# Performance work log

Hardware: AMD Instinct MI355X
Metric: run time of the kernel (lower is better)

## Reference

```python
import jax, jax.numpy as jnp
import numpy as np

N_KERNELS = 5
MUL_FACTOR = 2.0
# 2.0 ** (arange(5) - 2) = [0.25, 0.5, 1, 2, 4]
BANDWIDTH_MULTIPLIERS = MUL_FACTOR ** (np.arange(N_KERNELS) - N_KERNELS // 2)


def setup_inputs() -> dict:
    key = jax.random.key(0)
    kx, ky = jax.random.split(key)
    X = jax.random.normal(kx, (4096, 256), dtype=jnp.float32)
    Y = jax.random.normal(ky, (4096, 256), dtype=jnp.float32)
    return {"X": X, "Y": Y}


def _pairwise_sq_dists(Z):
    # ||z_i - z_j||^2 via GEMM; clamp tiny negatives from roundoff.
    sq = jnp.sum(Z * Z, axis=-1)  # [2N]
    d2 = sq[:, None] + sq[None, :] - 2.0 * (Z @ Z.T)  # [2N, 2N]
    return jnp.maximum(d2, 0.0)


def reference(X, Y):
    n = X.shape[0]
    Z = jnp.concatenate([X, Y], axis=0)  # [2N, D]
    d2 = _pairwise_sq_dists(Z)  # [2N, 2N]
    n_samples = d2.shape[0]
    # bandwidth uses .data in torch -> detached
    bandwidth = jax.lax.stop_gradient(d2.sum()) / (n_samples ** 2 - n_samples)
    mults = jnp.asarray(BANDWIDTH_MULTIPLIERS, dtype=d2.dtype)  # [5]
    # K = sum_k exp(-d2 / (bandwidth * mult_k))
    K = jnp.exp(-d2[None, :, :] / (bandwidth * mults)[:, None, None]).sum(axis=0)
    XX = K[:n, :n].mean()
    XY = K[:n, n:].mean()
    YY = K[n:, n:].mean()
    return XX - 2.0 * XY + YY
```

## Files before the change

### kernel.cpp

```cpp
#include <hip/hip_runtime.h>
#include <math.h>


#define N_HALF 4096
#define DIM 256
#define M_TOT 8192
#define TILE 128
#define NT 64
#define NT_HALF 32
#define CHUNK 4
#define NCHUNK 520

typedef unsigned short ushort_t;
typedef __attribute__((ext_vector_type(8))) short short8;
typedef __attribute__((ext_vector_type(4))) float floatx4;

__device__ ushort_t g_zf[M_TOT * DIM];

__device__ __forceinline__ ushort_t f2bf(float f) {
    unsigned u = __float_as_uint(f);
    u += 0x7fffu + ((u >> 16) & 1u);
    return (ushort_t)(u >> 16);
}

__device__ __forceinline__ void gload_lds16(const ushort_t* g, ushort_t* l) {
    __builtin_amdgcn_global_load_lds(
        (const __attribute__((address_space(1))) void*)g,
        (__attribute__((address_space(3))) void*)l, 16, 0, 0);
}

__device__ __forceinline__ void stage_slice(const ushort_t* gA, const ushort_t* gB,
                                            ushort_t* lA, ushort_t* lB,
                                            int wave, int lane) {
#pragma unroll
    for (int i = 0; i < 2; ++i) {
        const int c = wave * 2 + i;
        gload_lds16(gA + (size_t)c * 4096 + lane * 8, lA + c * 512);
        gload_lds16(gB + (size_t)c * 4096 + lane * 8, lB + c * 512);
    }
}

__device__ __forceinline__ void compute_kk(const ushort_t* lA, const ushort_t* lB,
                                           int a0, int b0, int laneoff,
                                           floatx4 (&accv)[4][4]) {
    short8 af[4], bf[4];
#pragma unroll
    for (int mi = 0; mi < 4; ++mi)
        af[mi] = *(const short8*)(lA + (a0 + mi) * 512 + laneoff);
#pragma unroll
    for (int ni = 0; ni < 4; ++ni)
        bf[ni] = *(const short8*)(lB + (b0 + ni) * 512 + laneoff);
#pragma unroll
    for (int mi = 0; mi < 4; ++mi)
#pragma unroll
        for (int ni = 0; ni < 4; ++ni)
            accv[mi][ni] = __builtin_amdgcn_mfma_f32_16x16x32_bf16(
                af[mi], bf[ni], accv[mi][ni], 0, 0, 0);
}

__global__ __launch_bounds__(256) void k_prep(const float* __restrict__ X,
                                              const float* __restrict__ Y,
                                              float* __restrict__ sq,
                                              float* __restrict__ colsum_r,
                                              float* __restrict__ Ssum_r) {
    __shared__ float cpart[4][256];
    __shared__ float spart[4];
    const int t = threadIdx.x, wave = t >> 6, lane = t & 63;
    const int row0 = blockIdx.x * 16 + wave * 4;
    const int kk = lane >> 3, q = (lane >> 1) & 3, j0 = (lane & 1) * 4;
    float c0 = 0.f, c1 = 0.f, c2 = 0.f, c3 = 0.f, ssum = 0.f;
#pragma unroll
    for (int i = 0; i < 4; ++i) {
        const int row = row0 + i;
        const float* p = (row < N_HALF) ? (X + (size_t)row * DIM)
                                        : (Y + (size_t)(row - N_HALF) * DIM);
        const float4 v = *((const float4*)p + lane);
        ushort4 hi;
        hi.x = f2bf(v.x); hi.y = f2bf(v.y); hi.z = f2bf(v.z); hi.w = f2bf(v.w);
        const int rb = row >> 4, m = row & 15;
        *(ushort4*)(g_zf + (size_t)rb * 4096 + kk * 512 + m * 32 + q * 8 + j0) = hi;
        c0 += v.x; c1 += v.y; c2 += v.z; c3 += v.w;
        float s = fmaf(v.x, v.x, fmaf(v.y, v.y, fmaf(v.z, v.z, v.w * v.w)));
#pragma unroll
        for (int off = 32; off > 0; off >>= 1) s += __shfl_xor(s, off);
        if (lane == 0) sq[row] = s;
        ssum += s;
    }
    float4 cp; cp.x = c0; cp.y = c1; cp.z = c2; cp.w = c3;
    *(float4*)&cpart[wave][lane * 4] = cp;
    if (lane == 0) spart[wave] = ssum;
    __syncthreads();
    const float cs = cpart[0][t] + cpart[1][t] + cpart[2][t] + cpart[3][t];
    const int rep = blockIdx.x & 7;
    atomicAdd(&colsum_r[rep * 256 + t], cs);
    if (t == 0) atomicAdd(&Ssum_r[rep], spart[0] + spart[1] + spart[2] + spart[3]);
}

__global__ __launch_bounds__(256) void k_bw(const float* __restrict__ colsum_r,
                                            const float* __restrict__ Ssum_r,
                                            float* __restrict__ c2out) {
    __shared__ double sred[4];
    const int t = threadIdx.x, lane = t & 63, wave = t >> 6;
    float csf = 0.f;
#pragma unroll
    for (int r = 0; r < 8; ++r) csf += colsum_r[r * 256 + t];
    double p = (double)csf * (double)csf;
#pragma unroll
    for (int off = 32; off > 0; off >>= 1) p += __shfl_xor(p, off);
    if (lane == 0) sred[wave] = p;
    __syncthreads();
    if (t == 0) {
        const double SS = sred[0] + sred[1] + sred[2] + sred[3];
        float Sf = 0.f;
#pragma unroll
        for (int r = 0; r < 8; ++r) Sf += Ssum_r[r];
        const double sum_d2 = 2.0 * (double)M_TOT * (double)Sf - 2.0 * SS;
        const double bw = sum_d2 / ((double)M_TOT * (double)M_TOT - (double)M_TOT);
        c2out[0] = (float)(1.4426950408889634 / (4.0 * bw));
    }
}

__global__ __launch_bounds__(256, 2) void k_gram(const float* __restrict__ sq,
                                                 const float* __restrict__ c2p,
                                                 double* __restrict__ acc,
                                                 unsigned* __restrict__ cnt,
                                                 float* __restrict__ out) {
    __shared__ __attribute__((aligned(16))) ushort_t lds[2][8192];
    __shared__ double redw[4][3];

    const int bid = (int)blockIdx.x;
    const int cc = (bid & 7) * 65 + (bid >> 3);
    const int f0 = cc * CHUNK;

    const int t = threadIdx.x;
    const int lane = t & 63, wave = t >> 6;
    const int l15 = lane & 15, quad = lane >> 4;
    const int wrow = (wave >> 1) * 64, wcol = (wave & 1) * 64;
    const int a0 = (wave >> 1) * 4, b0 = (wave & 1) * 4;
    const int laneoff = l15 * 32 + quad * 8;

    const float c2 = c2p[0];
    const float twoc2 = 2.f * c2;

    int ti = (int)((129.0f - sqrtf(16641.0f - 8.0f * (float)f0)) * 0.5f);
    if (ti < 0) ti = 0; if (ti > NT - 1) ti = NT - 1;
    while (ti * NT - ti * (ti - 1) / 2 > f0) --ti;
    while ((ti + 1) * NT - (ti + 1) * ti / 2 <= f0) ++ti;
    int tj = ti + (f0 - (ti * NT - ti * (ti - 1) / 2));

    const ushort_t* cgA = g_zf + (size_t)ti * 8 * 4096;
    const ushort_t* cgB = g_zf + (size_t)tj * 8 * 4096;

    stage_slice(cgA, cgB, lds[0], lds[0] + 4096, wave, lane);
    __syncthreads();

    double lxx = 0.0, lxy = 0.0, lyy = 0.0;
    int cur = 0;

#pragma unroll 1
    for (int s = 0; s < CHUNK; ++s) {
        int nti = ti, ntj = tj + 1;
        if (ntj == NT) { ++nti; ntj = nti; }
        const ushort_t* ngA = g_zf + (size_t)nti * 8 * 4096;
        const ushort_t* ngB = g_zf + (size_t)ntj * 8 * 4096;

        floatx4 accv[4][4];
#pragma unroll
        for (int mi = 0; mi < 4; ++mi)
#pragma unroll
            for (int ni = 0; ni < 4; ++ni) accv[mi][ni] = (floatx4)0.f;

#pragma unroll
        for (int kk = 0; kk < 8; ++kk) {
            if (kk < 7)
                stage_slice(cgA + (kk + 1) * 512, cgB + (kk + 1) * 512,
                            lds[cur ^ 1], lds[cur ^ 1] + 4096, wave, lane);
            else if (s < CHUNK - 1)
                stage_slice(ngA, ngB,
                            lds[cur ^ 1], lds[cur ^ 1] + 4096, wave, lane);
            compute_kk(lds[cur], lds[cur] + 4096, a0, b0, laneoff, accv);
            __syncthreads();
            cur ^= 1;
        }

        const int arow0 = ti * TILE, brow0 = tj * TILE;
        float nsj[4];
#pragma unroll
        for (int ni = 0; ni < 4; ++ni)
            nsj[ni] = -c2 * sq[brow0 + wcol + ni * 16 + l15];
        floatx4 nsi4[4];
#pragma unroll
        for (int mi = 0; mi < 4; ++mi) {
            const float4 sv = *(const float4*)&sq[arow0 + wrow + mi * 16 + quad * 4];
            nsi4[mi][0] = -c2 * sv.x; nsi4[mi][1] = -c2 * sv.y;
            nsi4[mi][2] = -c2 * sv.z; nsi4[mi][3] = -c2 * sv.w;
        }
        floatx4 sum4 = (floatx4)0.f;
#pragma unroll
        for (int mi = 0; mi < 4; ++mi) {
#pragma unroll
            for (int ni = 0; ni < 4; ++ni) {
                const floatx4 addv = nsi4[mi] + (floatx4)nsj[ni];
                floatx4 arg = twoc2 * accv[mi][ni] + addv;
                floatx4 tt;
#pragma unroll
                for (int r = 0; r < 4; ++r) tt[r] = exp2f(fminf(arg[r], 0.f));
                const floatx4 t2 = tt * tt, t4 = t2 * t2, t8 = t4 * t4, t16 = t8 * t8;
                sum4 += (tt + t2) + (t4 + t8) + t16;
            }
        }
        const float fsum = (sum4[0] + sum4[1]) + (sum4[2] + sum4[3]);
        const double contrib = ((ti == tj) ? 1.0 : 2.0) * (double)fsum;
        if (tj < NT_HALF)       lxx += contrib;
        else if (ti < NT_HALF)  lxy += contrib;
        else                    lyy += contrib;

        ti = nti; tj = ntj; cgA = ngA; cgB = ngB;
    }

#pragma unroll
    for (int off = 32; off > 0; off >>= 1) {
        lxx += __shfl_xor(lxx, off);
        lxy += __shfl_xor(lxy, off);
        lyy += __shfl_xor(lyy, off);
    }
    if (lane == 0) { redw[wave][0] = lxx; redw[wave][1] = lxy; redw[wave][2] = lyy; }
    __syncthreads();
    if (t == 0) {
        double sxx = 0.0, sxy = 0.0, syy = 0.0;
#pragma unroll
        for (int wv = 0; wv < 4; ++wv) {
            sxx += redw[wv][0]; sxy += redw[wv][1]; syy += redw[wv][2];
        }
        if (sxx != 0.0) atomicAdd(&acc[0], sxx);
        if (sxy != 0.0) atomicAdd(&acc[1], sxy);
        if (syy != 0.0) atomicAdd(&acc[2], syy);
        __threadfence();
        const unsigned old = atomicAdd(cnt, 1u);
        if (old == (0xAAAAAAAAu + (unsigned)(NCHUNK - 1)) ||
            old == (unsigned)(NCHUNK - 1)) {
            const double xx = atomicAdd(&acc[0], 0.0);
            const double xy = atomicAdd(&acc[1], 0.0);
            const double yy = atomicAdd(&acc[2], 0.0);
            out[0] = (float)((xx + yy - xy) *
                             (1.0 / ((double)N_HALF * (double)N_HALF)));
        }
    }
}

extern "C" void kernel_launch(void* const* d_in, const int* in_sizes, int n_in,
                              void* d_out, int out_size, void* d_ws, size_t ws_size,
                              hipStream_t stream) {
    const float* X = (const float*)d_in[0];
    const float* Y = (const float*)d_in[1];
    char* ws = (char*)d_ws;
    float* sq        = (float*)ws;
    float* colsum_r  = (float*)(ws + 32768);
    float* Ssum_r    = (float*)(ws + 40960);
    unsigned* cnt    = (unsigned*)(ws + 40992);
    double* acc      = (double*)(ws + 41000);
    float* c2ws      = (float*)(ws + 41024);
    float* out = (float*)d_out;

    hipLaunchKernelGGL(k_prep, dim3(512), dim3(256), 0, stream,
                       X, Y, sq, colsum_r, Ssum_r);
    hipLaunchKernelGGL(k_bw, dim3(1), dim3(256), 0, stream,
                       colsum_r, Ssum_r, c2ws);
    hipLaunchKernelGGL(k_gram, dim3(NCHUNK), dim3(256), 0, stream,
                       sq, c2ws, acc, cnt, out);
}
```

Baseline: 117.7 us.

## Stage two K-slices per barrier, swizzle bf16 layout, rebalance tile chunks

The Gram kernel now stages two K-slices (double-size LDS buffers) per pipeline step, which halves the number of __syncthreads barriers per tile. The packed bf16 layout of Z is reordered (q-major inside each slice), with the matching LDS read offset, presumably to cut LDS bank conflicts on the MFMA fragment loads. Work is redistributed over 512 blocks, some handling 5 tiles instead of 4, so the grid divides evenly across CUs. The cost is double the LDS footprint, which may reduce occupancy, and a small load imbalance from the 5-tile blocks.

```diff
diff --git a/kernel.cpp b/kernel.cpp
--- a/kernel.cpp
+++ b/kernel.cpp
@@ -8,8 +8,7 @@
 #define TILE 128
 #define NT 64
 #define NT_HALF 32
-#define CHUNK 4
-#define NCHUNK 520
+#define NCHUNK 512
 
 typedef unsigned short ushort_t;
 typedef __attribute__((ext_vector_type(8))) short short8;
@@ -29,14 +28,19 @@
         (__attribute__((address_space(3))) void*)l, 16, 0, 0);
 }
 
-__device__ __forceinline__ void stage_slice(const ushort_t* gA, const ushort_t* gB,
-                                            ushort_t* lA, ushort_t* lB,
-                                            int wave, int lane) {
-#pragma unroll
-    for (int i = 0; i < 2; ++i) {
-        const int c = wave * 2 + i;
-        gload_lds16(gA + (size_t)c * 4096 + lane * 8, lA + c * 512);
-        gload_lds16(gB + (size_t)c * 4096 + lane * 8, lB + c * 512);
+__device__ __forceinline__ void stage_slice2(const ushort_t* gA, const ushort_t* gB,
+                                             ushort_t* buf, int kk0,
+                                             int wave, int lane) {
+#pragma unroll
+    for (int s = 0; s < 2; ++s) {
+#pragma unroll
+        for (int i = 0; i < 2; ++i) {
+            const int c = wave * 2 + i;
+            gload_lds16(gA + (size_t)c * 4096 + (kk0 + s) * 512 + lane * 8,
+                        buf + s * 4096 + c * 512);
+            gload_lds16(gB + (size_t)c * 4096 + (kk0 + s) * 512 + lane * 8,
+                        buf + 8192 + s * 4096 + c * 512);
+        }
     }
 }
 
@@ -78,7 +82,7 @@
         ushort4 hi;
         hi.x = f2bf(v.x); hi.y = f2bf(v.y); hi.z = f2bf(v.z); hi.w = f2bf(v.w);
         const int rb = row >> 4, m = row & 15;
-        *(ushort4*)(g_zf + (size_t)rb * 4096 + kk * 512 + m * 32 + q * 8 + j0) = hi;
+        *(ushort4*)(g_zf + (size_t)rb * 4096 + kk * 512 + q * 128 + m * 8 + j0) = hi;
         c0 += v.x; c1 += v.y; c2 += v.z; c3 += v.w;
         float s = fmaf(v.x, v.x, fmaf(v.y, v.y, fmaf(v.z, v.z, v.w * v.w)));
 #pragma unroll
@@ -125,19 +129,20 @@
                                                  double* __restrict__ acc,
                                                  unsigned* __restrict__ cnt,
                                                  float* __restrict__ out) {
-    __shared__ __attribute__((aligned(16))) ushort_t lds[2][8192];
+    __shared__ __attribute__((aligned(16))) ushort_t lds[2][16384];
     __shared__ double redw[4][3];
 
     const int bid = (int)blockIdx.x;
-    const int cc = (bid & 7) * 65 + (bid >> 3);
-    const int f0 = cc * CHUNK;
+    const int cc = (bid & 7) * 64 + (bid >> 3);
+    const int nst = ((cc & 15) == 0) ? 5 : 4;
+    const int f0 = cc * 4 + ((cc + 15) >> 4);
 
     const int t = threadIdx.x;
     const int lane = t & 63, wave = t >> 6;
     const int l15 = lane & 15, quad = lane >> 4;
     const int wrow = (wave >> 1) * 64, wcol = (wave & 1) * 64;
     const int a0 = (wave >> 1) * 4, b0 = (wave & 1) * 4;
-    const int laneoff = l15 * 32 + quad * 8;
+    const int laneoff = quad * 128 + l15 * 8;
 
     const float c2 = c2p[0];
     const float twoc2 = 2.f * c2;
@@ -151,14 +156,14 @@
     const ushort_t* cgA = g_zf + (size_t)ti * 8 * 4096;
     const ushort_t* cgB = g_zf + (size_t)tj * 8 * 4096;
 
-    stage_slice(cgA, cgB, lds[0], lds[0] + 4096, wave, lane);
+    stage_slice2(cgA, cgB, lds[0], 0, wave, lane);
     __syncthreads();
 
     double lxx = 0.0, lxy = 0.0, lyy = 0.0;
     int cur = 0;
 
 #pragma unroll 1
-    for (int s = 0; s < CHUNK; ++s) {
+    for (int s = 0; s < nst; ++s) {
         int nti = ti, ntj = tj + 1;
         if (ntj == NT) { ++nti; ntj = nti; }
         const ushort_t* ngA = g_zf + (size_t)nti * 8 * 4096;
@@ -171,14 +176,14 @@
             for (int ni = 0; ni < 4; ++ni) accv[mi][ni] = (floatx4)0.f;
 
 #pragma unroll
-        for (int kk = 0; kk < 8; ++kk) {
-            if (kk < 7)
-                stage_slice(cgA + (kk + 1) * 512, cgB + (kk + 1) * 512,
-                            lds[cur ^ 1], lds[cur ^ 1] + 4096, wave, lane);
-            else if (s < CHUNK - 1)
-                stage_slice(ngA, ngB,
-                            lds[cur ^ 1], lds[cur ^ 1] + 4096, wave, lane);
-            compute_kk(lds[cur], lds[cur] + 4096, a0, b0, laneoff, accv);
+        for (int kk2 = 0; kk2 < 4; ++kk2) {
+            if (kk2 < 3)
+                stage_slice2(cgA, cgB, lds[cur ^ 1], (kk2 + 1) * 2, wave, lane);
+            else if (s < nst - 1)
+                stage_slice2(ngA, ngB, lds[cur ^ 1], 0, wave, lane);
+            compute_kk(lds[cur], lds[cur] + 8192, a0, b0, laneoff, accv);
+            compute_kk(lds[cur] + 4096, lds[cur] + 8192 + 4096,
+                       a0, b0, laneoff, accv);
             __syncthreads();
             cur ^= 1;
         }
```

Measured after the change: 115.5 us. About the same (-1.9%).
